# Kernel optimization log

Measured on AMD Instinct MI355X. Metric: run time of the kernel, lower is better.

The kernel has to match this reference:

```python
import jax, jax.numpy as jnp
import numpy as np

N_SEGMENT = 8
PATCH = 7          # correlation patch_size
RAD = PATCH // 2   # 3
EPS = 1e-5


def _bn(x, g, b):
    """BatchNorm (training-mode batch stats), channel axis = 1."""
    axes = tuple(i for i in range(x.ndim) if i != 1)
    m = x.mean(axes, keepdims=True)
    v = x.var(axes, keepdims=True)
    shp = [1] * x.ndim
    shp[1] = -1
    return (x - m) / jnp.sqrt(v + EPS) * g.reshape(shp) + b.reshape(shp)


def setup_inputs() -> dict:
    key = jax.random.key(0)
    ks = jax.random.split(key, 3)
    nt, c, h, w = 64, 64, 56, 56
    c_mid = c // 4                      # reduction=4 -> 16
    kk = PATCH * PATCH                  # corr_group=1 -> 49
    x = jax.random.normal(ks[0], (nt, c, h, w), dtype=jnp.float32)
    w21 = jax.random.normal(ks[1], (c_mid, c), dtype=jnp.float32) * (2.0 / c) ** 0.5
    w22 = jax.random.normal(ks[2], (c, kk), dtype=jnp.float32) * (2.0 / kk) ** 0.5
    return {
        "x": x, "w21": w21, "w22": w22,
        "g21": jnp.ones(c_mid), "b21": jnp.zeros(c_mid),
        "g22": jnp.ones(kk), "b22": jnp.zeros(kk),
        "g23": jnp.ones(c), "b23": jnp.zeros(c),
    }


def reference(x, w21, w22, g21, b21, g22, b22, g23, b23):
    nt, c, h, w = x.shape
    B = nt // N_SEGMENT
    residual = x

    # [B, c, T, h, w]
    xv = x.reshape(B, N_SEGMENT, c, h, w).transpose(0, 2, 1, 3, 4)
    # conv21: 1x1x1, c -> c_mid, no bias
    y = jnp.einsum('bcthw,oc->bothw', xv, w21)
    y = jax.nn.relu(_bn(y, g21, b21))          # [B, c_mid, T, h, w]

    # temporal shift: frame t pairs with frame t+1 (last with itself)
    idx = np.concatenate([np.arange(1, N_SEGMENT), [N_SEGMENT - 1]])
    y2 = y[:, :, idx]

    c_mid = y.shape[1]
    a = y.transpose(0, 2, 1, 3, 4).reshape(nt, c_mid, h, w)
    b2 = y2.transpose(0, 2, 1, 3, 4).reshape(nt, c_mid, h, w)

    # 7x7 local correlation (zero-padded), out[n, dy*7+dx, y, x] =
    #   sum_c a[n,c,y,x] * b2[n,c,y+dy-3,x+dx-3]
    bpad = jnp.pad(b2, ((0, 0), (0, 0), (RAD, RAD), (RAD, RAD)))
    corrs = [
        (a * bpad[:, :, dy:dy + h, dx:dx + w]).sum(axis=1)
        for dy in range(PATCH) for dx in range(PATCH)
    ]
    corr = jnp.stack(corrs, axis=1) / c_mid     # [nt, 49, h, w]

    corr = jax.nn.relu(_bn(corr, g22, b22))
    out = jnp.einsum('nkhw,ok->nohw', corr, w22)  # conv22: 1x1, 49 -> c
    out = _bn(out, g23, b23) + residual
    out = jax.nn.relu(out)
    return out  # net is identity
```

## Files before the change

### kernel.cpp

```cpp
#include <hip/hip_runtime.h>

#define HW 3136
#define W_ 56
#define C_IN 64
#define C_MID 16
#define KK 49
#define NT 64
#define NPIX (NT*HW)
#define NF 200704.0f

__global__ __launch_bounds__(256) void k1_conv(const float* __restrict__ x,
                                               const float* __restrict__ w21,
                                               float* __restrict__ y,
                                               float* __restrict__ st ) {
  float s[C_MID], q[C_MID];
#pragma unroll
  for (int o = 0; o < C_MID; ++o) { s[o] = 0.f; q[o] = 0.f; }

  for (int pix = blockIdx.x * 256 + threadIdx.x; pix < NPIX; pix += gridDim.x * 256) {
    int n = pix / HW; int hw = pix - n * HW;
    const float* xp = x + (size_t)n * C_IN * HW + hw;
    float acc[C_MID];
#pragma unroll
    for (int o = 0; o < C_MID; ++o) acc[o] = 0.f;
#pragma unroll
    for (int cb = 0; cb < C_IN; cb += 16) {
      float xv[16];
#pragma unroll
      for (int j = 0; j < 16; ++j) xv[j] = xp[(cb + j) * HW];
#pragma unroll
      for (int o = 0; o < C_MID; ++o) {
        float a = acc[o];
#pragma unroll
        for (int j = 0; j < 16; ++j) a = fmaf(w21[o * C_IN + cb + j], xv[j], a);
        acc[o] = a;
      }
    }
    float* yp = y + (size_t)n * C_MID * HW + hw;
#pragma unroll
    for (int o = 0; o < C_MID; ++o) {
      yp[o * HW] = acc[o];
      s[o] += acc[o];
      q[o] += acc[o] * acc[o];
    }
  }

  __shared__ float combS[C_MID][4], combQ[C_MID][4];
  int wv = threadIdx.x >> 6;
  int lane = threadIdx.x & 63;
#pragma unroll
  for (int o = 0; o < C_MID; ++o) {
    float a = s[o], b = q[o];
#pragma unroll
    for (int off = 32; off > 0; off >>= 1) {
      a += __shfl_xor(a, off, 64);
      b += __shfl_xor(b, off, 64);
    }
    if (lane == 0) { combS[o][wv] = a; combQ[o][wv] = b; }
  }
  __syncthreads();
  if (threadIdx.x < 32) {
    int o = threadIdx.x & 15;
    float t = (threadIdx.x < 16)
      ? (combS[o][0] + combS[o][1] + combS[o][2] + combS[o][3])
      : (combQ[o][0] + combQ[o][1] + combQ[o][2] + combQ[o][3]);
    atomicAdd(&st[threadIdx.x], t);
  }
}

__global__ void k_fin(const float* __restrict__ s, const float* __restrict__ q,
                      const float* __restrict__ g, const float* __restrict__ b,
                      float* __restrict__ sc, float* __restrict__ sh, int C) {
  int i = threadIdx.x;
  if (i < C) {
    float m = s[i] * (1.0f / NF);
    float v = q[i] * (1.0f / NF) - m * m;
    float inv = g[i] / sqrtf(v + 1e-5f);
    sc[i] = inv;
    sh[i] = fmaf(-m, inv, b[i]);
  }
}

#define HR 14
#define HC 62
#define HSZ (HR*HC)
__global__ __launch_bounds__(448) void k3_corr(const float* __restrict__ y,
                                               const float* __restrict__ sc1,
                                               const float* __restrict__ sh1,
                                               float* __restrict__ corr) {
  __shared__ float Bl[C_MID * HSZ];
  int tid = threadIdx.x;
  int n = blockIdx.x / 7;
  int rt = blockIdx.x - n * 7;
  int r0 = rt * 8;
  int t = n & 7;
  int n2 = (n & ~7) | (t < 7 ? t + 1 : 7);

  const float* yb = y + (size_t)n2 * C_MID * HW;
  for (int idx = tid; idx < C_MID * HSZ; idx += 448) {
    int c = idx / HSZ; int rem = idx - c * HSZ;
    int rr = rem / HC; int cc = rem - rr * HC;
    int gr = r0 + rr - 3; int gc = cc - 3;
    float v = 0.f;
    if (gr >= 0 && gr < 56 && gc >= 0 && gc < 56) {
      v = yb[c * HW + gr * W_ + gc];
      v = fmaxf(fmaf(sc1[c], v, sh1[c]), 0.f);
    }
    Bl[idx] = v;
  }

  int ty = tid / W_; int tx = tid - ty * W_;
  int r = r0 + ty;
  float a[C_MID];
  const float* ya = y + (size_t)n * C_MID * HW + r * W_ + tx;
#pragma unroll
  for (int c = 0; c < C_MID; ++c)
    a[c] = fmaxf(fmaf(sc1[c], ya[c * HW], sh1[c]), 0.f);

  __syncthreads();

  float* cp = corr + (size_t)n * KK * HW + r * W_ + tx;
#pragma unroll
  for (int dy = 0; dy < 7; ++dy) {
#pragma unroll
    for (int dx = 0; dx < 7; ++dx) {
      const float* bp = Bl + (ty + dy) * HC + (tx + dx);
      float v0 = 0.f, v1 = 0.f;
#pragma unroll
      for (int c = 0; c < C_MID; c += 2) {
        v0 = fmaf(a[c],     bp[c * HSZ],       v0);
        v1 = fmaf(a[c + 1], bp[(c + 1) * HSZ], v1);
      }
      cp[(dy * 7 + dx) * HW] = (v0 + v1) * (1.0f / 16.0f);
    }
  }
}

__global__ __launch_bounds__(256) void k3b_stats(const float* __restrict__ corr,
                                                 float* __restrict__ st ) {
  const float* base = corr + (size_t)blockIdx.x * HW;
  int k = blockIdx.x % KK;
  float s = 0.f, q = 0.f;
  const float4* b4 = (const float4*)base;
  for (int i = threadIdx.x; i < HW / 4; i += 256) {
    float4 v = b4[i];
    s += v.x + v.y + v.z + v.w;
    q += v.x * v.x + v.y * v.y + v.z * v.z + v.w * v.w;
  }
#pragma unroll
  for (int off = 32; off > 0; off >>= 1) {
    s += __shfl_xor(s, off, 64);
    q += __shfl_xor(q, off, 64);
  }
  __shared__ float rs[4], rq[4];
  int wv = threadIdx.x >> 6; int lane = threadIdx.x & 63;
  if (lane == 0) { rs[wv] = s; rq[wv] = q; }
  __syncthreads();
  if (threadIdx.x == 0) {
    atomicAdd(&st[k],      rs[0] + rs[1] + rs[2] + rs[3]);
    atomicAdd(&st[KK + k], rq[0] + rq[1] + rq[2] + rq[3]);
  }
}

__global__ __launch_bounds__(256) void k5_mat(const float* __restrict__ corr,
                                              const float* __restrict__ sc2,
                                              const float* __restrict__ sh2,
                                              const float* __restrict__ w22,
                                              float* __restrict__ tt) {
  int pix = blockIdx.x * 256 + threadIdx.x;
  int n = pix / HW; int hw = pix - n * HW;
  const float* cp = corr + (size_t)n * KK * HW + hw;
  float cr[KK];
#pragma unroll
  for (int k = 0; k < KK; ++k)
    cr[k] = fmaxf(fmaf(sc2[k], cp[k * HW], sh2[k]), 0.f);

  float* tp = tt + (size_t)n * C_IN * HW + hw;
#pragma unroll 4
  for (int o = 0; o < 64; ++o) {
    const float* wr = w22 + o * KK;
    float t0 = 0.f, t1 = 0.f, t2 = 0.f, t3 = 0.f;
#pragma unroll
    for (int k = 0; k < 48; k += 4) {
      t0 = fmaf(wr[k],     cr[k],     t0);
      t1 = fmaf(wr[k + 1], cr[k + 1], t1);
      t2 = fmaf(wr[k + 2], cr[k + 2], t2);
      t3 = fmaf(wr[k + 3], cr[k + 3], t3);
    }
    t0 = fmaf(wr[48], cr[48], t0);
    tp[o * HW] = (t0 + t1) + (t2 + t3);
  }
}

__global__ __launch_bounds__(256) void k5b_stats(const float* __restrict__ tt,
                                                 float* __restrict__ st ) {
  const float4* b4 = (const float4*)(tt + (size_t)blockIdx.x * HW);
  int o = blockIdx.x & 63;
  float s = 0.f, q = 0.f;
  for (int i = threadIdx.x; i < HW / 4; i += 256) {
    float4 v = b4[i];
    s += v.x + v.y + v.z + v.w;
    q += v.x * v.x + v.y * v.y + v.z * v.z + v.w * v.w;
  }
#pragma unroll
  for (int off = 32; off > 0; off >>= 1) {
    s += __shfl_xor(s, off, 64);
    q += __shfl_xor(q, off, 64);
  }
  __shared__ float rs[4], rq[4];
  int wv = threadIdx.x >> 6; int lane = threadIdx.x & 63;
  if (lane == 0) { rs[wv] = s; rq[wv] = q; }
  __syncthreads();
  if (threadIdx.x == 0) {
    atomicAdd(&st[o],      rs[0] + rs[1] + rs[2] + rs[3]);
    atomicAdd(&st[64 + o], rq[0] + rq[1] + rq[2] + rq[3]);
  }
}

__global__ __launch_bounds__(256) void k7_ew(const float* __restrict__ tt,
                                             const float* __restrict__ sc3,
                                             const float* __restrict__ sh3,
                                             const float* __restrict__ x,
                                             float* __restrict__ out) {
  const int tot4 = NPIX * C_IN / 4;
  const float4* t4 = (const float4*)tt;
  const float4* x4 = (const float4*)x;
  float4* o4 = (float4*)out;
  for (int i = blockIdx.x * 256 + threadIdx.x; i < tot4; i += gridDim.x * 256) {
    int plane = i / (HW / 4);
    int o = plane & 63;
    float a = sc3[o], b = sh3[o];
    float4 t = t4[i];
    float4 xv = x4[i];
    float4 r;
    r.x = fmaxf(fmaf(a, t.x, b) + xv.x, 0.f);
    r.y = fmaxf(fmaf(a, t.y, b) + xv.y, 0.f);
    r.z = fmaxf(fmaf(a, t.z, b) + xv.z, 0.f);
    r.w = fmaxf(fmaf(a, t.w, b) + xv.w, 0.f);
    o4[i] = r;
  }
}

__global__ __launch_bounds__(256) void k5_stats(const float* __restrict__ corr,
                                                const float* __restrict__ sc2,
                                                const float* __restrict__ sh2,
                                                const float* __restrict__ w22,
                                                float* __restrict__ s3, float* __restrict__ q3) {
  __shared__ float aS[64], aQ[64];
  if (threadIdx.x < 64) { aS[threadIdx.x] = 0.f; aQ[threadIdx.x] = 0.f; }
  __syncthreads();
  int lane = threadIdx.x & 63;
  for (int pix = blockIdx.x * 256 + threadIdx.x; pix < NPIX; pix += gridDim.x * 256) {
    int n = pix / HW; int hw = pix - n * HW;
    const float* cp = corr + (size_t)n * KK * HW + hw;
    float cr[KK];
#pragma unroll
    for (int k = 0; k < KK; ++k)
      cr[k] = fmaxf(fmaf(sc2[k], cp[k * HW], sh2[k]), 0.f);
    for (int o = 0; o < 64; ++o) {
      const float* wr = w22 + o * KK;
      float t0 = 0.f, t1 = 0.f, t2 = 0.f, t3 = 0.f;
#pragma unroll
      for (int k = 0; k < 48; k += 4) {
        t0 = fmaf(wr[k],     cr[k],     t0);
        t1 = fmaf(wr[k + 1], cr[k + 1], t1);
        t2 = fmaf(wr[k + 2], cr[k + 2], t2);
        t3 = fmaf(wr[k + 3], cr[k + 3], t3);
      }
      t0 = fmaf(wr[48], cr[48], t0);
      float ttv = (t0 + t1) + (t2 + t3);
      float vs = ttv, vq = ttv * ttv;
#pragma unroll
      for (int off = 32; off > 0; off >>= 1) {
        vs += __shfl_xor(vs, off, 64);
        vq += __shfl_xor(vq, off, 64);
      }
      if (lane == 0) { atomicAdd(&aS[o], vs); atomicAdd(&aQ[o], vq); }
    }
  }
  __syncthreads();
  if (threadIdx.x < 64) {
    atomicAdd(&s3[threadIdx.x], aS[threadIdx.x]);
    atomicAdd(&q3[threadIdx.x], aQ[threadIdx.x]);
  }
}

__global__ __launch_bounds__(256) void k7_out(const float* __restrict__ corr,
                                              const float* __restrict__ sc2,
                                              const float* __restrict__ sh2,
                                              const float* __restrict__ w22,
                                              const float* __restrict__ sc3,
                                              const float* __restrict__ sh3,
                                              const float* __restrict__ x,
                                              float* __restrict__ out) {
  for (int pix = blockIdx.x * 256 + threadIdx.x; pix < NPIX; pix += gridDim.x * 256) {
    int n = pix / HW; int hw = pix - n * HW;
    const float* cp = corr + (size_t)n * KK * HW + hw;
    float cr[KK];
#pragma unroll
    for (int k = 0; k < KK; ++k)
      cr[k] = fmaxf(fmaf(sc2[k], cp[k * HW], sh2[k]), 0.f);
    const float* xp = x + (size_t)n * C_IN * HW + hw;
    float* op = out + (size_t)n * C_IN * HW + hw;
#pragma unroll 4
    for (int o = 0; o < 64; ++o) {
      const float* wr = w22 + o * KK;
      float t0 = 0.f, t1 = 0.f, t2 = 0.f, t3 = 0.f;
#pragma unroll
      for (int k = 0; k < 48; k += 4) {
        t0 = fmaf(wr[k],     cr[k],     t0);
        t1 = fmaf(wr[k + 1], cr[k + 1], t1);
        t2 = fmaf(wr[k + 2], cr[k + 2], t2);
        t3 = fmaf(wr[k + 3], cr[k + 3], t3);
      }
      t0 = fmaf(wr[48], cr[48], t0);
      float ttv = (t0 + t1) + (t2 + t3);
      float r = fmaf(sc3[o], ttv, sh3[o]) + xp[o * HW];
      op[o * HW] = fmaxf(r, 0.f);
    }
  }
}

extern "C" void kernel_launch(void* const* d_in, const int* in_sizes, int n_in,
                              void* d_out, int out_size, void* d_ws, size_t ws_size,
                              hipStream_t stream) {
  const float* x   = (const float*)d_in[0];
  const float* w21 = (const float*)d_in[1];
  const float* w22 = (const float*)d_in[2];
  const float* g21 = (const float*)d_in[3];
  const float* b21 = (const float*)d_in[4];
  const float* g22 = (const float*)d_in[5];
  const float* b22 = (const float*)d_in[6];
  const float* g23 = (const float*)d_in[7];
  const float* b23 = (const float*)d_in[8];
  float* out = (float*)d_out;

  const size_t Y_F    = (size_t)NT * C_MID * HW;
  const size_t CORR_F = (size_t)NT * KK * HW;
  const size_t TT_F   = (size_t)NT * C_IN * HW;
  const size_t ST_F   = 1024;

  float* ws   = (float*)d_ws;
  float* y    = ws;
  float* corr = y + Y_F;
  float* st   = corr + CORR_F;
  float* tt   = st + ST_F;

  float* s1 = st;        float* q1 = s1 + 16;
  float* s2 = q1 + 16;   float* q2 = s2 + KK;
  float* s3 = q2 + KK;   float* q3 = s3 + 64;
  float* sc1 = st + 300; float* sh1 = sc1 + 16;
  float* sc2 = sh1 + 16; float* sh2 = sc2 + KK;
  float* sc3 = sh2 + KK; float* sh3 = sc3 + 64;

  bool fast = ws_size >= (Y_F + CORR_F + ST_F + TT_F) * sizeof(float);

  hipMemsetAsync(st, 0, 258 * sizeof(float), stream);

  k1_conv  <<<512, 256, 0, stream>>>(x, w21, y, s1);
  k_fin    <<<1,   64,  0, stream>>>(s1, q1, g21, b21, sc1, sh1, C_MID);
  k3_corr  <<<448, 448, 0, stream>>>(y, sc1, sh1, corr);
  k3b_stats<<<NT * KK, 256, 0, stream>>>(corr, s2);
  k_fin    <<<1,   64,  0, stream>>>(s2, q2, g22, b22, sc2, sh2, KK);

  if (fast) {
    k5_mat  <<<NPIX / 256, 256, 0, stream>>>(corr, sc2, sh2, w22, tt);
    k5b_stats<<<NT * C_IN, 256, 0, stream>>>(tt, s3);
    k_fin   <<<1,   64,  0, stream>>>(s3, q3, g23, b23, sc3, sh3, C_IN);
    k7_ew   <<<2048, 256, 0, stream>>>(tt, sc3, sh3, x, out);
  } else {
    k5_stats<<<512, 256, 0, stream>>>(corr, sc2, sh2, w22, s3, q3);
    k_fin   <<<1,   64,  0, stream>>>(s3, q3, g23, b23, sc3, sh3, C_IN);
    k7_out  <<<1024, 256, 0, stream>>>(corr, sc2, sh2, w22, sc3, sh3, x, out);
  }
}
```

Baseline: 305.6 us.

## Fold BN finalize into consumer kernels and pack conv21 output as float2

Removes the three tiny k_fin launches on the fast path by recomputing BatchNorm scale/shift inside k3_corr, k5_mat and k7_ew from the accumulated stats. Stores the conv21 output channel-pair interleaved as float2 so the correlation kernel loads and reads shared memory with 8-byte accesses. The correlation kernel is retiled to 7-row tiles with 392 threads and 512 blocks, and k1_conv's grid goes from 512 to 784 blocks. Occupancy hints are added to the matmul kernels. In exchange, every block redoes the small finalize computation.

After: 294.1 us. -3.8%, faster.

```diff
diff --git a/kernel.cpp b/kernel.cpp
--- a/kernel.cpp
+++ b/kernel.cpp
@@ -8,10 +8,11 @@
 #define NT 64
 #define NPIX (NT*HW)
 #define NF 200704.0f
+#define EPS 1e-5f
 
 __global__ __launch_bounds__(256) void k1_conv(const float* __restrict__ x,
                                                const float* __restrict__ w21,
-                                               float* __restrict__ y,
+                                               float2* __restrict__ y2,
                                                float* __restrict__ st ) {
   float s[C_MID], q[C_MID];
 #pragma unroll
@@ -36,10 +37,13 @@
         acc[o] = a;
       }
     }
-    float* yp = y + (size_t)n * C_MID * HW + hw;
+    float2* yp = y2 + (size_t)n * 8 * HW + hw;
+#pragma unroll
+    for (int c2 = 0; c2 < 8; ++c2) {
+      yp[c2 * HW] = make_float2(acc[2 * c2], acc[2 * c2 + 1]);
+    }
 #pragma unroll
     for (int o = 0; o < C_MID; ++o) {
-      yp[o * HW] = acc[o];
       s[o] += acc[o];
       q[o] += acc[o] * acc[o];
     }
@@ -75,47 +79,67 @@
   if (i < C) {
     float m = s[i] * (1.0f / NF);
     float v = q[i] * (1.0f / NF) - m * m;
-    float inv = g[i] / sqrtf(v + 1e-5f);
+    float inv = g[i] / sqrtf(v + EPS);
     sc[i] = inv;
     sh[i] = fmaf(-m, inv, b[i]);
   }
 }
 
-#define HR 14
+#define TR 7
+#define HR 13
 #define HC 62
-#define HSZ (HR*HC)
-__global__ __launch_bounds__(448) void k3_corr(const float* __restrict__ y,
-                                               const float* __restrict__ sc1,
-                                               const float* __restrict__ sh1,
+#define HSZ2 (HR*HC)
+__global__ __launch_bounds__(392) void k3_corr(const float2* __restrict__ y2,
+                                               const float* __restrict__ st ,
+                                               const float* __restrict__ g21,
+                                               const float* __restrict__ b21,
                                                float* __restrict__ corr) {
-  __shared__ float Bl[C_MID * HSZ];
+  __shared__ float2 Bl[8 * HSZ2];
+  __shared__ float4 bn1[8];
   int tid = threadIdx.x;
-  int n = blockIdx.x / 7;
-  int rt = blockIdx.x - n * 7;
-  int r0 = rt * 8;
+  int n = blockIdx.x >> 3;
+  int rt = blockIdx.x & 7;
+  int r0 = rt * TR;
   int t = n & 7;
   int n2 = (n & ~7) | (t < 7 ? t + 1 : 7);
 
-  const float* yb = y + (size_t)n2 * C_MID * HW;
-  for (int idx = tid; idx < C_MID * HSZ; idx += 448) {
-    int c = idx / HSZ; int rem = idx - c * HSZ;
+  if (tid < 8) {
+    int cA = 2 * tid, cB = 2 * tid + 1;
+    float mA = st[cA] * (1.0f / NF), mB = st[cB] * (1.0f / NF);
+    float vA = st[16 + cA] * (1.0f / NF) - mA * mA;
+    float vB = st[16 + cB] * (1.0f / NF) - mB * mB;
+    float iA = g21[cA] / sqrtf(vA + EPS);
+    float iB = g21[cB] / sqrtf(vB + EPS);
+    bn1[tid] = make_float4(iA, fmaf(-mA, iA, b21[cA]), iB, fmaf(-mB, iB, b21[cB]));
+  }
+  __syncthreads();
+
+  const float2* yb = y2 + (size_t)n2 * 8 * HW;
+  for (int idx = tid; idx < 8 * HSZ2; idx += 392) {
+    int c2 = idx / HSZ2; int rem = idx - c2 * HSZ2;
     int rr = rem / HC; int cc = rem - rr * HC;
     int gr = r0 + rr - 3; int gc = cc - 3;
-    float v = 0.f;
+    float2 v = make_float2(0.f, 0.f);
     if (gr >= 0 && gr < 56 && gc >= 0 && gc < 56) {
-      v = yb[c * HW + gr * W_ + gc];
-      v = fmaxf(fmaf(sc1[c], v, sh1[c]), 0.f);
+      float2 raw = yb[c2 * HW + gr * W_ + gc];
+      float4 p = bn1[c2];
+      v.x = fmaxf(fmaf(p.x, raw.x, p.y), 0.f);
+      v.y = fmaxf(fmaf(p.z, raw.y, p.w), 0.f);
     }
     Bl[idx] = v;
   }
 
   int ty = tid / W_; int tx = tid - ty * W_;
   int r = r0 + ty;
-  float a[C_MID];
-  const float* ya = y + (size_t)n * C_MID * HW + r * W_ + tx;
-#pragma unroll
-  for (int c = 0; c < C_MID; ++c)
-    a[c] = fmaxf(fmaf(sc1[c], ya[c * HW], sh1[c]), 0.f);
+  float2 a2[8];
+  const float2* ya = y2 + (size_t)n * 8 * HW + r * W_ + tx;
+#pragma unroll
+  for (int c2 = 0; c2 < 8; ++c2) {
+    float2 raw = ya[c2 * HW];
+    float4 p = bn1[c2];
+    a2[c2] = make_float2(fmaxf(fmaf(p.x, raw.x, p.y), 0.f),
+                         fmaxf(fmaf(p.z, raw.y, p.w), 0.f));
+  }
 
   __syncthreads();
 
@@ -124,12 +148,13 @@
   for (int dy = 0; dy < 7; ++dy) {
 #pragma unroll
     for (int dx = 0; dx < 7; ++dx) {
-      const float* bp = Bl + (ty + dy) * HC + (tx + dx);
+      const float2* bp = Bl + (ty + dy) * HC + (tx + dx);
       float v0 = 0.f, v1 = 0.f;
 #pragma unroll
-      for (int c = 0; c < C_MID; c += 2) {
-        v0 = fmaf(a[c],     bp[c * HSZ],       v0);
-        v1 = fmaf(a[c + 1], bp[(c + 1) * HSZ], v1);
+      for (int c2 = 0; c2 < 8; ++c2) {
+        float2 bv = bp[c2 * HSZ2];
+        v0 = fmaf(a2[c2].x, bv.x, v0);
+        v1 = fmaf(a2[c2].y, bv.y, v1);
       }
       cp[(dy * 7 + dx) * HW] = (v0 + v1) * (1.0f / 16.0f);
     }
@@ -162,18 +187,30 @@
   }
 }
 
-__global__ __launch_bounds__(256) void k5_mat(const float* __restrict__ corr,
-                                              const float* __restrict__ sc2,
-                                              const float* __restrict__ sh2,
-                                              const float* __restrict__ w22,
-                                              float* __restrict__ tt) {
+__global__ __launch_bounds__(256, 3) void k5_mat(const float* __restrict__ corr,
+                                                 const float* __restrict__ st ,
+                                                 const float* __restrict__ g22,
+                                                 const float* __restrict__ b22,
+                                                 const float* __restrict__ w22,
+                                                 float* __restrict__ tt) {
+  __shared__ float bsc[KK], bsh[KK];
+  if (threadIdx.x < KK) {
+    int k = threadIdx.x;
+    float m = st[k] * (1.0f / NF);
+    float v = st[KK + k] * (1.0f / NF) - m * m;
+    float inv = g22[k] / sqrtf(v + EPS);
+    bsc[k] = inv;
+    bsh[k] = fmaf(-m, inv, b22[k]);
+  }
+  __syncthreads();
+
   int pix = blockIdx.x * 256 + threadIdx.x;
   int n = pix / HW; int hw = pix - n * HW;
   const float* cp = corr + (size_t)n * KK * HW + hw;
   float cr[KK];
 #pragma unroll
   for (int k = 0; k < KK; ++k)
-    cr[k] = fmaxf(fmaf(sc2[k], cp[k * HW], sh2[k]), 0.f);
+    cr[k] = fmaxf(fmaf(bsc[k], cp[k * HW], bsh[k]), 0.f);
 
   float* tp = tt + (size_t)n * C_IN * HW + hw;
 #pragma unroll 4
@@ -218,10 +255,22 @@
 }
 
 __global__ __launch_bounds__(256) void k7_ew(const float* __restrict__ tt,
-                                             const float* __restrict__ sc3,
-                                             const float* __restrict__ sh3,
+                                             const float* __restrict__ st ,
+                                             const float* __restrict__ g23,
+                                             const float* __restrict__ b23,
                                              const float* __restrict__ x,
                                              float* __restrict__ out) {
+  __shared__ float csc[64], csh[64];
+  if (threadIdx.x < 64) {
+    int o = threadIdx.x;
+    float m = st[o] * (1.0f / NF);
+    float v = st[64 + o] * (1.0f / NF) - m * m;
+    float inv = g23[o] / sqrtf(v + EPS);
+    csc[o] = inv;
+    csh[o] = fmaf(-m, inv, b23[o]);
+  }
+  __syncthreads();
+
   const int tot4 = NPIX * C_IN / 4;
   const float4* t4 = (const float4*)tt;
   const float4* x4 = (const float4*)x;
@@ -229,7 +278,7 @@
   for (int i = blockIdx.x * 256 + threadIdx.x; i < tot4; i += gridDim.x * 256) {
     int plane = i / (HW / 4);
     int o = plane & 63;
-    float a = sc3[o], b = sh3[o];
+    float a = csc[o], b = csh[o];
     float4 t = t4[i];
     float4 xv = x4[i];
     float4 r;
@@ -241,11 +290,11 @@
   }
 }
 
-__global__ __launch_bounds__(256) void k5_stats(const float* __restrict__ corr,
-                                                const float* __restrict__ sc2,
-                                                const float* __restrict__ sh2,
-                                                const float* __restrict__ w22,
-                                                float* __restrict__ s3, float* __restrict__ q3) {
+__global__ __launch_bounds__(256, 3) void k5_stats(const float* __restrict__ corr,
+                                                   const float* __restrict__ sc2,
+                                                   const float* __restrict__ sh2,
+                                                   const float* __restrict__ w22,
+                                                   float* __restrict__ s3, float* __restrict__ q3) {
   __shared__ float aS[64], aQ[64];
   if (threadIdx.x < 64) { aS[threadIdx.x] = 0.f; aQ[threadIdx.x] = 0.f; }
   __syncthreads();
@@ -285,14 +334,14 @@
   }
 }
 
-__global__ __launch_bounds__(256) void k7_out(const float* __restrict__ corr,
-                                              const float* __restrict__ sc2,
-                                              const float* __restrict__ sh2,
-                                              const float* __restrict__ w22,
-                                              const float* __restrict__ sc3,
-                                              const float* __restrict__ sh3,
-                                              const float* __restrict__ x,
-                                              float* __restrict__ out) {
+__global__ __launch_bounds__(256, 3) void k7_out(const float* __restrict__ corr,
+                                                 const float* __restrict__ sc2,
+                                                 const float* __restrict__ sh2,
+                                                 const float* __restrict__ w22,
+                                                 const float* __restrict__ sc3,
+                                                 const float* __restrict__ sh3,
+                                                 const float* __restrict__ x,
+                                                 float* __restrict__ out) {
   for (int pix = blockIdx.x * 256 + threadIdx.x; pix < NPIX; pix += gridDim.x * 256) {
     int n = pix / HW; int hw = pix - n * HW;
     const float* cp = corr + (size_t)n * KK * HW + hw;
@@ -341,36 +390,33 @@
   const size_t ST_F   = 1024;
 
   float* ws   = (float*)d_ws;
-  float* y    = ws;
-  float* corr = y + Y_F;
+  float2* y2  = (float2*)ws;
+  float* corr = ws + Y_F;
   float* st   = corr + CORR_F;
   float* tt   = st + ST_F;
 
-  float* s1 = st;        float* q1 = s1 + 16;
-  float* s2 = q1 + 16;   float* q2 = s2 + KK;
-  float* s3 = q2 + KK;   float* q3 = s3 + 64;
-  float* sc1 = st + 300; float* sh1 = sc1 + 16;
-  float* sc2 = sh1 + 16; float* sh2 = sc2 + KK;
-  float* sc3 = sh2 + KK; float* sh3 = sc3 + 64;
+  float* s1 = st;          float* q1 = s1 + 16;
+  float* s2 = q1 + 16;     float* q2 = s2 + KK;
+  float* s3 = q2 + KK;     float* q3 = s3 + 64;
+  float* sc2 = st + 300;   float* sh2 = sc2 + KK;
+  float* sc3 = sh2 + KK;   float* sh3 = sc3 + 64;
 
   bool fast = ws_size >= (Y_F + CORR_F + ST_F + TT_F) * sizeof(float);
 
   hipMemsetAsync(st, 0, 258 * sizeof(float), stream);
 
-  k1_conv  <<<512, 256, 0, stream>>>(x, w21, y, s1);
-  k_fin    <<<1,   64,  0, stream>>>(s1, q1, g21, b21, sc1, sh1, C_MID);
-  k3_corr  <<<448, 448, 0, stream>>>(y, sc1, sh1, corr);
+  k1_conv  <<<784, 256, 0, stream>>>(x, w21, y2, s1);
+  k3_corr  <<<512, 392, 0, stream>>>(y2, s1, g21, b21, corr);
   k3b_stats<<<NT * KK, 256, 0, stream>>>(corr, s2);
-  k_fin    <<<1,   64,  0, stream>>>(s2, q2, g22, b22, sc2, sh2, KK);
 
   if (fast) {
-    k5_mat  <<<NPIX / 256, 256, 0, stream>>>(corr, sc2, sh2, w22, tt);
+    k5_mat   <<<NPIX / 256, 256, 0, stream>>>(corr, s2, g22, b22, w22, tt);
     k5b_stats<<<NT * C_IN, 256, 0, stream>>>(tt, s3);
-    k_fin   <<<1,   64,  0, stream>>>(s3, q3, g23, b23, sc3, sh3, C_IN);
-    k7_ew   <<<2048, 256, 0, stream>>>(tt, sc3, sh3, x, out);
+    k7_ew    <<<2048, 256, 0, stream>>>(tt, s3, g23, b23, x, out);
   } else {
-    k5_stats<<<512, 256, 0, stream>>>(corr, sc2, sh2, w22, s3, q3);
-    k_fin   <<<1,   64,  0, stream>>>(s3, q3, g23, b23, sc3, sh3, C_IN);
-    k7_out  <<<1024, 256, 0, stream>>>(corr, sc2, sh2, w22, sc3, sh3, x, out);
-  }
-}
+    k_fin    <<<1, 64, 0, stream>>>(s2, q2, g22, b22, sc2, sh2, KK);
+    k5_stats <<<512, 256, 0, stream>>>(corr, sc2, sh2, w22, s3, q3);
+    k_fin    <<<1, 64, 0, stream>>>(s3, q3, g23, b23, sc3, sh3, C_IN);
+    k7_out   <<<1024, 256, 0, stream>>>(corr, sc2, sh2, w22, sc3, sh3, x, out);
+  }
+}
```
